# Kernel tuning notes

Measured on AMD Instinct MI355X. Metric: run time of the kernel, lower is better.

The kernel has to match this reference:

```python
import jax, jax.numpy as jnp
import numpy as np

WIN = 3  # win_size from init


def setup_inputs() -> dict:
    key = jax.random.key(0)
    ks = jax.random.split(key, 7)
    B, H, W, d = 8, 128, 128, 128
    N = H * W
    s = d ** -0.5  # param init scale
    return {
        "x": jax.random.normal(ks[0], (B, N, d), dtype=jnp.float32),
        "Wq": jax.random.normal(ks[1], (d, d), dtype=jnp.float32) * s,
        "bq": jax.random.normal(ks[2], (d,), dtype=jnp.float32) * 0.01,
        "Wk": jax.random.normal(ks[3], (d, d), dtype=jnp.float32) * s,
        "bk": jax.random.normal(ks[4], (d,), dtype=jnp.float32) * 0.01,
        "Wv": jax.random.normal(ks[5], (d, d), dtype=jnp.float32) * s,
        "bv": jax.random.normal(ks[6], (d,), dtype=jnp.float32) * 0.01,
        "H": H,
        "W": W,
    }


def reference(x, Wq, bq, Wk, bk, Wv, bv, H, W):
    B, N, d = x.shape
    scale = d ** -0.5
    pad = WIN // 2

    q = (x @ Wq + bq).reshape(B, H, W, d)
    k = (x @ Wk + bk).reshape(B, H, W, d)
    v = (x @ Wv + bv).reshape(B, H, W, d)

    # zero-pad spatial dims (matches F.pad); padded neighbors get logit 0, not -inf
    k_pad = jnp.pad(k, ((0, 0), (pad, pad), (pad, pad), (0, 0)))
    v_pad = jnp.pad(v, ((0, 0), (pad, pad), (pad, pad), (0, 0)))

    scores_l, vs_l = [], []
    for dy in range(WIN):
        for dx in range(WIN):
            k_slice = k_pad[:, dy:dy + H, dx:dx + W]   # [B,H,W,d]
            v_slice = v_pad[:, dy:dy + H, dx:dx + W]
            scores_l.append(jnp.einsum("bhwd,bhwd->bhw", q, k_slice) * scale)
            vs_l.append(v_slice)

    scores = jnp.stack(scores_l, axis=-1)            # [B,H,W,9]
    prob = jax.nn.softmax(scores, axis=-1)           # [B,H,W,9]
    v_stk = jnp.stack(vs_l, axis=-1)                 # [B,H,W,d,9]
    out = jnp.einsum("bhwn,bhwdn->bhwd", prob, v_stk)
    return out.reshape(B, N, d)
```

## Files before the change

### kernel.cpp

```cpp
#include <hip/hip_runtime.h>
#include <stdint.h>

#define B_ 8
#define H_ 128
#define W_ 128
#define D_ 128
#define N_ (H_*W_)
#define M_ (B_*N_)

typedef __attribute__((ext_vector_type(8))) short short8;
typedef __attribute__((ext_vector_type(4))) float floatx4;

typedef const __attribute__((address_space(1))) void* gas_t;
typedef __attribute__((address_space(3))) void* las_t;

__device__ inline unsigned short f2bf(float f){
  union { float f; unsigned int i; } c; c.f = f;
  unsigned int x = c.i;
  x += 0x7FFF + ((x >> 16) & 1);
  return (unsigned short)(x >> 16);
}
__device__ inline float bflo(unsigned int u){
  union { unsigned int i; float f; } c; c.i = u << 16; return c.f;
}
__device__ inline float bfhi(unsigned int u){
  union { unsigned int i; float f; } c; c.i = u & 0xFFFF0000u; return c.f;
}

__global__ void wtrans_kernel(const float* __restrict__ Wq, const float* __restrict__ Wk,
                              const float* __restrict__ Wv, unsigned short* __restrict__ Wt){
  const float* src = blockIdx.x == 0 ? Wq : (blockIdx.x == 1 ? Wk : Wv);
  unsigned short* dst = Wt + blockIdx.x * (D_*D_);
  const int i = blockIdx.y * 256 + threadIdx.x;
  const int k = i >> 7, n = i & 127;
  dst[n*D_ + k] = f2bf(src[i]);
}

__global__ __launch_bounds__(256, 2) void qkv_gemm_kernel(
    const float* __restrict__ x, const unsigned short* __restrict__ Wt,
    const float* __restrict__ bq, const float* __restrict__ bk, const float* __restrict__ bv,
    unsigned short* __restrict__ Q, unsigned short* __restrict__ K, unsigned short* __restrict__ V)
{
  const int rowTile = blockIdx.x;

  __shared__ unsigned short lds[16384];

  const int t = threadIdx.x;
  const int wave = t >> 6, lane = t & 63;
  const int m0 = lane & 15, quad = lane >> 4;
  const int wm = (wave >> 1) * 64, wn = (wave & 1) * 64;

  {
    #pragma unroll
    for (int p = 0; p < 8; ++p){
      int s = p*256 + t;
      int n = s >> 4, cp = s & 15, c = cp ^ (n & 7);
      __builtin_amdgcn_global_load_lds((gas_t)(const void*)(Wt + n*128 + c*8),
                                       (las_t)(void*)((unsigned short*)lds + p*2048 + wave*512),
                                       16, 0, 0);
    }
  }

  short8 a[4][4];
  const float* xbase = x + (size_t)(rowTile*128 + wm + m0) * D_ + quad*8;
  #pragma unroll
  for (int half = 0; half < 2; ++half){
    float4 f[8][2];
    #pragma unroll
    for (int kk2 = 0; kk2 < 2; ++kk2)
      #pragma unroll
      for (int i = 0; i < 4; ++i){
        const float* gp = xbase + i*16*D_ + (half*2 + kk2)*32;
        f[kk2*4+i][0] = *(const float4*)gp;
        f[kk2*4+i][1] = *(const float4*)(gp + 4);
      }
    #pragma unroll
    for (int kk2 = 0; kk2 < 2; ++kk2)
      #pragma unroll
      for (int i = 0; i < 4; ++i){
        short8 v;
        v[0] = (short)f2bf(f[kk2*4+i][0].x);
        v[1] = (short)f2bf(f[kk2*4+i][0].y);
        v[2] = (short)f2bf(f[kk2*4+i][0].z);
        v[3] = (short)f2bf(f[kk2*4+i][0].w);
        v[4] = (short)f2bf(f[kk2*4+i][1].x);
        v[5] = (short)f2bf(f[kk2*4+i][1].y);
        v[6] = (short)f2bf(f[kk2*4+i][1].z);
        v[7] = (short)f2bf(f[kk2*4+i][1].w);
        a[half*2 + kk2][i] = v;
      }
  }
  __syncthreads();

  #pragma unroll
  for (int which = 0; which < 3; ++which){
    floatx4 acc[4][4] = {};
    #pragma unroll
    for (int kk = 0; kk < 4; ++kk){
      short8 b[4];
      #pragma unroll
      for (int j = 0; j < 4; ++j){
        int n = wn + j*16 + m0;
        int c = (kk*4 + quad) ^ (n & 7);
        b[j] = *(const short8*)&lds[n*128 + c*8];
      }
      #pragma unroll
      for (int j = 0; j < 4; ++j)
        #pragma unroll
        for (int i = 0; i < 4; ++i)
          acc[j][i] = __builtin_amdgcn_mfma_f32_16x16x32_bf16(b[j], a[kk][i], acc[j][i], 0, 0, 0);
    }

    {
      const float* bias = which == 0 ? bq : (which == 1 ? bk : bv);
      unsigned short* Out = which == 0 ? Q : (which == 1 ? K : V);
      unsigned short* Outp = Out + (size_t)rowTile * 128 * D_;
      #pragma unroll
      for (int j = 0; j < 4; ++j){
        const float4 bb = *(const float4*)&bias[wn + j*16 + quad*4];
        #pragma unroll
        for (int i = 0; i < 4; ++i){
          const int row = wm + i*16 + m0;
          uint2 pk;
          pk.x = (unsigned)f2bf(acc[j][i][0] + bb.x) | ((unsigned)f2bf(acc[j][i][1] + bb.y) << 16);
          pk.y = (unsigned)f2bf(acc[j][i][2] + bb.z) | ((unsigned)f2bf(acc[j][i][3] + bb.w) << 16);
          *(uint2*)(Outp + row*D_ + wn + j*16 + quad*4) = pk;
        }
      }
    }

    if (which < 2){
      __syncthreads();
      const unsigned short* Wnext = Wt + (which + 1) * (D_*D_);
      #pragma unroll
      for (int p = 0; p < 8; ++p){
        int s = p*256 + t;
        int n = s >> 4, cp = s & 15, c = cp ^ (n & 7);
        __builtin_amdgcn_global_load_lds((gas_t)(const void*)(Wnext + n*128 + c*8),
                                         (las_t)(void*)((unsigned short*)lds + p*2048 + wave*512),
                                         16, 0, 0);
      }
      __syncthreads();
    }
  }
}

__global__ __launch_bounds__(256, 2) void attn_kernel(
    const unsigned short* __restrict__ Q, const unsigned short* __restrict__ K,
    const unsigned short* __restrict__ V, float* __restrict__ out)
{
  const int t = threadIdx.x;
  const int e8 = t & 7;
  const int pix = blockIdx.x * 32 + (t >> 3);
  const int w = pix & 127;
  const int h = (pix >> 7) & 127;
  const int bbase = pix & ~(N_ - 1);
  const float scale = 0.08838834764831845f;
  const int doff = e8 * 16;
  const size_t off = (size_t)pix * D_ + doff;

  int npix[9]; bool okm[9];
  #pragma unroll
  for (int i = 0; i < 9; ++i){
    const int dy = i/3 - 1, dx = i%3 - 1;
    const int hh = h + dy, ww = w + dx;
    okm[i] = ((unsigned)hh < 128u) && ((unsigned)ww < 128u);
    const int hc = min(max(hh, 0), 127);
    const int wc = min(max(ww, 0), 127);
    npix[i] = bbase + hc*W_ + wc;
  }

  uint4 qu0, qu1;
  {
    const unsigned short* qp = Q + off;
    qu0 = *(const uint4*)qp;
    qu1 = *(const uint4*)(qp + 8);
  }
  uint4 ku[9][2];
  #pragma unroll
  for (int i = 0; i < 9; ++i){
    const unsigned short* kp = K + (size_t)npix[i]*D_ + doff;
    ku[i][0] = *(const uint4*)kp;
    ku[i][1] = *(const uint4*)(kp + 8);
  }
  uint4 vu[9][2];
  #pragma unroll
  for (int i = 0; i < 9; ++i){
    const unsigned short* vp = V + (size_t)npix[i]*D_ + doff;
    vu[i][0] = *(const uint4*)vp;
    vu[i][1] = *(const uint4*)(vp + 8);
  }

  float q[16];
  {
    unsigned uu[8] = {qu0.x, qu0.y, qu0.z, qu0.w, qu1.x, qu1.y, qu1.z, qu1.w};
    #pragma unroll
    for (int e = 0; e < 8; ++e){
      q[e*2]     = bflo(uu[e]) * scale;
      q[e*2 + 1] = bfhi(uu[e]) * scale;
    }
  }

  float s[9];
  #pragma unroll
  for (int i = 0; i < 9; ++i){
    unsigned uu[8] = {ku[i][0].x, ku[i][0].y, ku[i][0].z, ku[i][0].w,
                      ku[i][1].x, ku[i][1].y, ku[i][1].z, ku[i][1].w};
    float acc = 0.f;
    #pragma unroll
    for (int e = 0; e < 8; ++e){
      acc += q[e*2]     * bflo(uu[e]);
      acc += q[e*2 + 1] * bfhi(uu[e]);
    }
    s[i] = okm[i] ? acc : 0.f;
  }
  #pragma unroll
  for (int i = 0; i < 9; ++i){
    s[i] += __shfl_xor(s[i], 1, 64);
    s[i] += __shfl_xor(s[i], 2, 64);
    s[i] += __shfl_xor(s[i], 4, 64);
  }

  float m = s[0];
  #pragma unroll
  for (int i = 1; i < 9; ++i) m = fmaxf(m, s[i]);
  float p[9]; float l = 0.f;
  #pragma unroll
  for (int i = 0; i < 9; ++i){ p[i] = __expf(s[i] - m); l += p[i]; }
  const float inv = 1.f / l;

  float o[16];
  #pragma unroll
  for (int d = 0; d < 16; ++d) o[d] = 0.f;
  #pragma unroll
  for (int i = 0; i < 9; ++i){
    const float pi = okm[i] ? p[i] * inv : 0.f;
    unsigned uu[8] = {vu[i][0].x, vu[i][0].y, vu[i][0].z, vu[i][0].w,
                      vu[i][1].x, vu[i][1].y, vu[i][1].z, vu[i][1].w};
    #pragma unroll
    for (int e = 0; e < 8; ++e){
      o[e*2]     += pi * bflo(uu[e]);
      o[e*2 + 1] += pi * bfhi(uu[e]);
    }
  }

  float* op = out + off;
  #pragma unroll
  for (int c = 0; c < 4; ++c){
    float4 v4 = make_float4(o[c*4], o[c*4+1], o[c*4+2], o[c*4+3]);
    *(float4*)(op + c*4) = v4;
  }
}

extern "C" void kernel_launch(void* const* d_in, const int* in_sizes, int n_in,
                              void* d_out, int out_size, void* d_ws, size_t ws_size,
                              hipStream_t stream)
{
  const float* x  = (const float*)d_in[0];
  const float* Wq = (const float*)d_in[1];
  const float* bq = (const float*)d_in[2];
  const float* Wk = (const float*)d_in[3];
  const float* bk = (const float*)d_in[4];
  const float* Wv = (const float*)d_in[5];
  const float* bv = (const float*)d_in[6];
  float* out = (float*)d_out;

  char* ws = (char*)d_ws;
  unsigned short* Wt = (unsigned short*)ws;
  unsigned short* Q  = (unsigned short*)(ws + (1<<17));
  unsigned short* K  = (unsigned short*)(ws + (1<<17) + (size_t)M_*D_*2);
  unsigned short* V  = (unsigned short*)(ws + (1<<17) + (size_t)2*M_*D_*2);

  hipLaunchKernelGGL(wtrans_kernel, dim3(3, 64), dim3(256), 0, stream, Wq, Wk, Wv, Wt);
  hipLaunchKernelGGL(qkv_gemm_kernel, dim3(M_/128), dim3(256), 0, stream,
                     x, Wt, bq, bk, bv, Q, K, V);
  hipLaunchKernelGGL(attn_kernel, dim3(M_/32), dim3(256), 0, stream, Q, K, V, out);
}
```

Before: 202.6 us.

## Double-buffer weight tiles in QKV GEMM to overlap loads with MFMA compute

Doubles the LDS allocation so the next projection's weight tile is prefetched into a second buffer while the current one is used. Full __syncthreads are replaced with targeted s_waitcnt vmcnt counts plus barriers, and scheduling barriers are added. The aim is to hide global-to-LDS weight load latency between the Q, K and V GEMM phases. The cost is more LDS per block, which may reduce occupancy, and hand-counted vmcnt values that are fragile if the compiler reorders memory ops.

New measurement: 202.3 us. Within noise of the previous version (-0.2%).

```diff
diff --git a/kernel.cpp b/kernel.cpp
--- a/kernel.cpp
+++ b/kernel.cpp
@@ -36,6 +36,16 @@
   dst[n*D_ + k] = f2bf(src[i]);
 }
 
+__device__ __forceinline__ void stage_B(unsigned short* ldsbase, const unsigned short* Wsel,
+                                        int t, int wave){
+  #pragma unroll
+  for (int p = 0; p < 8; ++p){
+    int s = p*256 + t, n = s >> 4, cp = s & 15, c = cp ^ (n & 7);
+    __builtin_amdgcn_global_load_lds((gas_t)(const void*)(Wsel + n*128 + c*8),
+                                     (las_t)(void*)(ldsbase + p*2048 + wave*512), 16, 0, 0);
+  }
+}
+
 __global__ __launch_bounds__(256, 2) void qkv_gemm_kernel(
     const float* __restrict__ x, const unsigned short* __restrict__ Wt,
     const float* __restrict__ bq, const float* __restrict__ bk, const float* __restrict__ bv,
@@ -43,23 +53,14 @@
 {
   const int rowTile = blockIdx.x;
 
-  __shared__ unsigned short lds[16384];
+  __shared__ unsigned short lds[32768];
 
   const int t = threadIdx.x;
   const int wave = t >> 6, lane = t & 63;
   const int m0 = lane & 15, quad = lane >> 4;
   const int wm = (wave >> 1) * 64, wn = (wave & 1) * 64;
 
-  {
-    #pragma unroll
-    for (int p = 0; p < 8; ++p){
-      int s = p*256 + t;
-      int n = s >> 4, cp = s & 15, c = cp ^ (n & 7);
-      __builtin_amdgcn_global_load_lds((gas_t)(const void*)(Wt + n*128 + c*8),
-                                       (las_t)(void*)((unsigned short*)lds + p*2048 + wave*512),
-                                       16, 0, 0);
-    }
-  }
+  stage_B((unsigned short*)lds, Wt, t, wave);
 
   short8 a[4][4];
   const float* xbase = x + (size_t)(rowTile*128 + wm + m0) * D_ + quad*8;
@@ -74,6 +75,7 @@
         f[kk2*4+i][0] = *(const float4*)gp;
         f[kk2*4+i][1] = *(const float4*)(gp + 4);
       }
+    __builtin_amdgcn_sched_barrier(0);
     #pragma unroll
     for (int kk2 = 0; kk2 < 2; ++kk2)
       #pragma unroll
@@ -90,10 +92,17 @@
         a[half*2 + kk2][i] = v;
       }
   }
-  __syncthreads();
+
+  stage_B((unsigned short*)lds + 16384, Wt + D_*D_, t, wave);
+
+  asm volatile("s_waitcnt vmcnt(8)" ::: "memory");
+  __builtin_amdgcn_sched_barrier(0);
+  __builtin_amdgcn_s_barrier();
 
   #pragma unroll
   for (int which = 0; which < 3; ++which){
+    const int bufbase = (which & 1) ? 16384 : 0;
+
     floatx4 acc[4][4] = {};
     #pragma unroll
     for (int kk = 0; kk < 4; ++kk){
@@ -102,7 +111,7 @@
       for (int j = 0; j < 4; ++j){
         int n = wn + j*16 + m0;
         int c = (kk*4 + quad) ^ (n & 7);
-        b[j] = *(const short8*)&lds[n*128 + c*8];
+        b[j] = *(const short8*)&lds[bufbase + n*128 + c*8];
       }
       #pragma unroll
       for (int j = 0; j < 4; ++j)
@@ -129,18 +138,16 @@
       }
     }
 
-    if (which < 2){
-      __syncthreads();
-      const unsigned short* Wnext = Wt + (which + 1) * (D_*D_);
-      #pragma unroll
-      for (int p = 0; p < 8; ++p){
-        int s = p*256 + t;
-        int n = s >> 4, cp = s & 15, c = cp ^ (n & 7);
-        __builtin_amdgcn_global_load_lds((gas_t)(const void*)(Wnext + n*128 + c*8),
-                                         (las_t)(void*)((unsigned short*)lds + p*2048 + wave*512),
-                                         16, 0, 0);
-      }
-      __syncthreads();
+    if (which == 0){
+      __builtin_amdgcn_s_barrier();
+      stage_B((unsigned short*)lds, Wt + 2*(D_*D_), t, wave);
+      asm volatile("s_waitcnt vmcnt(24)" ::: "memory");
+      __builtin_amdgcn_sched_barrier(0);
+      __builtin_amdgcn_s_barrier();
+    } else if (which == 1){
+      asm volatile("s_waitcnt vmcnt(16)" ::: "memory");
+      __builtin_amdgcn_sched_barrier(0);
+      __builtin_amdgcn_s_barrier();
     }
   }
 }
```
